# Performance work log

Measured on AMD Instinct MI355X. Metric: run time of the kernel, lower is better.

The kernel has to match this reference:

```python
import jax, jax.numpy as jnp
import numpy as np

B, T, S, F, D, M = 8, 8192, 8192, 64, 64, 128
EPS = 1e-9


def _draw_omega(n_omega, d_feature, rng):
    # Stacked orthogonal blocks scaled by sqrt(d_feature), as in the TF module.
    n_blocks = (n_omega + d_feature - 1) // d_feature + 1
    blocks = []
    for _ in range(n_blocks):
        g = rng.standard_normal((d_feature, d_feature)).astype(np.float32)
        q, _ = np.linalg.qr(g)
        blocks.append(q * np.sqrt(float(d_feature)))
    return jnp.asarray(np.concatenate(blocks, axis=0)[:n_omega])


def setup_inputs() -> dict:
    k0 = jax.random.key(0)
    kq, kv, kk = jax.random.split(k0, 3)
    query = jax.random.normal(kq, (B, T, F), dtype=jnp.float32)
    value = jax.random.normal(kv, (B, S, D), dtype=jnp.float32)
    key = jax.random.normal(kk, (B, S, F), dtype=jnp.float32)
    omega = _draw_omega(M, F, np.random.default_rng(0))  # (M, F)
    return {"query": query, "value": value, "key": key, "omega": omega}


def _phi(x, omega):
    # x: (B, L, F) -> (B, L, 2M) positive random features
    m = omega.shape[0]
    square_sum = jnp.sum(x * x, axis=-1, keepdims=True) / 2.0  # (B, L, 1)
    xw = jnp.einsum('blf,mf->blm', x, omega)                   # (B, L, M)
    unnorm = jnp.exp(jnp.concatenate([xw, -xw], axis=-1) - square_sum) + EPS
    return unnorm / jnp.sqrt(2.0 * m)


def reference(query, value, key, omega):
    q = _phi(query, omega)  # (B, T, 2M)
    k = _phi(key, omega)    # (B, S, 2M)
    ones = jnp.ones(value.shape[:-1] + (1,), dtype=value.dtype)
    v1 = jnp.concatenate([value, ones], axis=-1)               # (B, S, D+1)
    kv = jnp.einsum('bsm,bsd->bmd', k, v1)                     # (B, 2M, D+1)
    qkv = jnp.einsum('btm,bmd->btd', q, kv)                    # (B, T, D+1)
    normalizer = qkv[:, :, -1:]
    return qkv[:, :, :-1] / normalizer
```

## Files before the change

kernel.cpp:

```cpp
#include <hip/hip_runtime.h>


constexpr int NB = 8;
constexpr int NT = 8192;
constexpr float EPSF = 1e-9f;
constexpr float SCALE = 0.0625f;

typedef short s8v __attribute__((ext_vector_type(8)));
typedef short s4v __attribute__((ext_vector_type(4)));
typedef float f4v __attribute__((ext_vector_type(4)));

__device__ inline f4v mfma16(s8v a, s8v b, f4v c) {
  return __builtin_amdgcn_mfma_f32_16x16x32_bf16(a, b, c, 0, 0, 0);
}

__device__ inline short bf16_rne(float f) {
  unsigned u = __builtin_bit_cast(unsigned, f);
  u += 0x7fffu + ((u >> 16) & 1u);
  return (short)(u >> 16);
}
__device__ inline float bf16_to_f(short h) {
  unsigned u = ((unsigned)(unsigned short)h) << 16;
  return __builtin_bit_cast(float, u);
}

__global__ void setup_omega(const float* __restrict__ omega,
                            short* __restrict__ oh, short* __restrict__ ol) {
  int i = blockIdx.x * 256 + threadIdx.x;
  if (i >= 128 * 64) return;
  float w = omega[i];
  short h = bf16_rne(w);
  oh[i] = h;
  ol[i] = bf16_rne(w - bf16_to_f(h));
}

struct PhiRows {
  s8v ah0, al0, ah1, al1;
  float ssr[4];
  float ss;
};

__device__ inline void split8(f4v a, f4v b, s8v& h, s8v& l) {
  float v[8] = {a.x, a.y, a.z, a.w, b.x, b.y, b.z, b.w};
#pragma unroll
  for (int j = 0; j < 8; ++j) {
    short hh = bf16_rne(v[j]);
    h[j] = hh;
    l[j] = bf16_rne(v[j] - bf16_to_f(hh));
  }
}

__device__ inline void load_phi_rows(const float* __restrict__ xrow_base, int lane, PhiRows& P) {
  const int r = lane & 15, q = lane >> 4;
  const float* p = xrow_base + r * 64 + q * 8;
  f4v u0 = *(const f4v*)(p);
  f4v u1 = *(const f4v*)(p + 4);
  f4v u2 = *(const f4v*)(p + 32);
  f4v u3 = *(const f4v*)(p + 36);
  float ss = u0.x * u0.x + u0.y * u0.y + u0.z * u0.z + u0.w * u0.w
           + u1.x * u1.x + u1.y * u1.y + u1.z * u1.z + u1.w * u1.w
           + u2.x * u2.x + u2.y * u2.y + u2.z * u2.z + u2.w * u2.w
           + u3.x * u3.x + u3.y * u3.y + u3.z * u3.z + u3.w * u3.w;
  ss += __shfl_xor(ss, 16, 64);
  ss += __shfl_xor(ss, 32, 64);
  ss *= 0.5f;
  P.ss = ss;
#pragma unroll
  for (int reg = 0; reg < 4; ++reg) P.ssr[reg] = __shfl(ss, q * 4 + reg, 64);
  split8(u0, u1, P.ah0, P.al0);
  split8(u2, u3, P.ah1, P.al1);
}

__device__ inline f4v phi_xw_tile(const PhiRows& P, const short* __restrict__ oh,
                                  const short* __restrict__ ol, int f0, int lane) {
  const int fr = f0 + (lane & 15);
  const int q = lane >> 4;
  s8v bh0 = *(const s8v*)(oh + fr * 64 + q * 8);
  s8v bh1 = *(const s8v*)(oh + fr * 64 + 32 + q * 8);
  s8v bl0 = *(const s8v*)(ol + fr * 64 + q * 8);
  s8v bl1 = *(const s8v*)(ol + fr * 64 + 32 + q * 8);
  f4v c = {0.f, 0.f, 0.f, 0.f};
  c = mfma16(P.ah0, bh0, c);
  c = mfma16(P.ah1, bh1, c);
  c = mfma16(P.al0, bh0, c);
  c = mfma16(P.al1, bh1, c);
  c = mfma16(P.ah0, bl0, c);
  c = mfma16(P.ah1, bl1, c);
  return c;
}

__device__ inline f4v phi_xw_tile_T(const PhiRows& P, const short* __restrict__ oh,
                                    const short* __restrict__ ol, int f0, int lane) {
  const int fr = f0 + (lane & 15);
  const int q = lane >> 4;
  s8v ah0 = *(const s8v*)(oh + fr * 64 + q * 8);
  s8v ah1 = *(const s8v*)(oh + fr * 64 + 32 + q * 8);
  s8v al0 = *(const s8v*)(ol + fr * 64 + q * 8);
  s8v al1 = *(const s8v*)(ol + fr * 64 + 32 + q * 8);
  f4v c = {0.f, 0.f, 0.f, 0.f};
  c = mfma16(ah0, P.ah0, c);
  c = mfma16(ah1, P.ah1, c);
  c = mfma16(al0, P.ah0, c);
  c = mfma16(al1, P.ah1, c);
  c = mfma16(ah0, P.al0, c);
  c = mfma16(ah1, P.al1, c);
  return c;
}

constexpr int KF_P = 72;

__global__ __launch_bounds__(256, 4) void kv_fused(
    const float* __restrict__ key, const float* __restrict__ value,
    const short* __restrict__ oh, const short* __restrict__ ol,
    float* __restrict__ partial, int use_partial) {
  __shared__ short kft[64 * KF_P];
  __shared__ short v1t[80 * KF_P];
  const int tid = threadIdx.x, lane = tid & 63, w = tid >> 6;
  const int b = blockIdx.x >> 8;
  const int cb = blockIdx.x & 255;
  const int chunk = cb >> 2, fq = cb & 3;
  const int s0 = chunk * 128;
  const int q = lane >> 4, r15 = lane & 15;

  for (int i = tid; i < 15 * KF_P; i += 256) v1t[65 * KF_P + i] = 0;

  f4v acc[5];
#pragma unroll
  for (int n = 0; n < 5; ++n) acc[n] = f4v{0.f, 0.f, 0.f, 0.f};

  for (int sc = 0; sc < 2; ++sc) {
    const int sbase = s0 + sc * 64;
    __syncthreads();
    {
      const float* vb = value + ((size_t)b * NT + sbase) * 64;
#pragma unroll
      for (int i = 0; i < 16; ++i) {
        int e = tid + i * 256;
        int s = e >> 6, d = e & 63;
        v1t[d * KF_P + s] = bf16_rne(vb[e]);
      }
      if (tid < 64) v1t[64 * KF_P + tid] = (short)0x3F80;
    }
    {
      PhiRows P;
      load_phi_rows(key + ((size_t)b * NT + sbase + w * 16) * 64, lane, P);
#pragma unroll
      for (int ft = 0; ft < 2; ++ft) {
        f4v c = phi_xw_tile(P, oh, ol, fq * 32 + ft * 16, lane);
        s4v pk, nk;
#pragma unroll
        for (int reg = 0; reg < 4; ++reg) {
          float xw = c[reg];
          pk[reg] = bf16_rne((__expf(xw - P.ssr[reg]) + EPSF) * SCALE);
          nk[reg] = bf16_rne((__expf(-xw - P.ssr[reg]) + EPSF) * SCALE);
        }
        const int scol = w * 16 + q * 4;
        *(s4v*)(kft + (ft * 16 + r15) * KF_P + scol) = pk;
        *(s4v*)(kft + (32 + ft * 16 + r15) * KF_P + scol) = nk;
      }
    }
    __syncthreads();
#pragma unroll
    for (int ks = 0; ks < 2; ++ks) {
      s8v a = *(const s8v*)(kft + (w * 16 + r15) * KF_P + ks * 32 + q * 8);
#pragma unroll
      for (int n = 0; n < 5; ++n) {
        s8v bf = *(const s8v*)(v1t + (n * 16 + r15) * KF_P + ks * 32 + q * 8);
        acc[n] = mfma16(a, bf, acc[n]);
      }
    }
  }
  if (use_partial) {
    float* pb = partial + (size_t)blockIdx.x * 5120;
#pragma unroll
    for (int n = 0; n < 5; ++n) {
      int d = n * 16 + r15;
      *(f4v*)(pb + d * 64 + w * 16 + q * 4) = acc[n];
    }
  } else {
    float* pb = partial + ((size_t)(b * 4 + fq)) * 5120;
#pragma unroll
    for (int n = 0; n < 5; ++n) {
      int d = n * 16 + r15;
#pragma unroll
      for (int reg = 0; reg < 4; ++reg)
        atomicAdd(pb + d * 64 + w * 16 + q * 4 + reg, acc[n][reg]);
    }
  }
}

__global__ __launch_bounds__(256) void kv_finalize(
    const float* __restrict__ src, short* __restrict__ kvfrag,
    int nchunks, size_t bstride) {
  int i = blockIdx.x * 256 + threadIdx.x;
  int b = i / 20480;
  int rem = i - b * 20480;
  int fid = rem >> 9;
  int lane = (rem >> 3) & 63;
  int j = rem & 7;
  int ks = fid / 5, n = fid - ks * 5;
  int r = lane & 15, q = lane >> 4;
  int d = n * 16 + r;
  int k = ks * 32 + q * 8 + j;
  int fq = (k >> 5) & 3;
  int lf = (k & 31) + ((k >> 7) << 5);
  const float* p = src + (size_t)b * bstride + fq * 5120 + d * 64 + lf;
  float s = 0.f;
#pragma unroll 8
  for (int c = 0; c < nchunks; ++c) s += p[(size_t)c * 20480];
  kvfrag[i] = bf16_rne(s);
}

constexpr int QF_P = 264;
__global__ __launch_bounds__(256, 4) void qkv_fused(
    const float* __restrict__ query, const short* __restrict__ oh,
    const short* __restrict__ ol, const short* __restrict__ kvfrag,
    float* __restrict__ out) {
  __shared__ __align__(16) short qf[64 * QF_P];
  const int tid = threadIdx.x, lane = tid & 63, w = tid >> 6;
  const int b = blockIdx.x >> 7;
  const int t0 = (blockIdx.x & 127) * 64;
  const int q = lane >> 4, r15 = lane & 15;

  {
    PhiRows P;
    load_phi_rows(query + ((size_t)b * NT + t0 + w * 16) * 64, lane, P);
    const int t_loc = w * 16 + r15;
#pragma unroll
    for (int ft = 0; ft < 8; ++ft) {
      f4v c = phi_xw_tile_T(P, oh, ol, ft * 16, lane);
      s4v pk, nk;
#pragma unroll
      for (int reg = 0; reg < 4; ++reg) {
        float xw = c[reg];
        pk[reg] = bf16_rne((__expf(xw - P.ss) + EPSF) * SCALE);
        nk[reg] = bf16_rne((__expf(-xw - P.ss) + EPSF) * SCALE);
      }
      *(s4v*)(qf + t_loc * QF_P + ft * 16 + q * 4) = pk;
      *(s4v*)(qf + t_loc * QF_P + 128 + ft * 16 + q * 4) = nk;
    }
  }
  __syncthreads();
  f4v acc[5];
#pragma unroll
  for (int n = 0; n < 5; ++n) acc[n] = f4v{0.f, 0.f, 0.f, 0.f};
  const short* kvb = kvfrag + (size_t)b * 40 * 512;
#pragma unroll
  for (int ks = 0; ks < 8; ++ks) {
    s8v a = *(const s8v*)(qf + (w * 16 + r15) * QF_P + ks * 32 + q * 8);
#pragma unroll
    for (int n = 0; n < 5; ++n) {
      s8v bf = *(const s8v*)(kvb + ((size_t)(ks * 5 + n)) * 512 + lane * 8);
      acc[n] = mfma16(a, bf, acc[n]);
    }
  }
  float den_r[4];
#pragma unroll
  for (int reg = 0; reg < 4; ++reg) den_r[reg] = __shfl(acc[4][reg], lane & 48, 64);
  float* stg = (float*)(qf + w * 16 * QF_P);
#pragma unroll
  for (int n = 0; n < 4; ++n)
#pragma unroll
    for (int reg = 0; reg < 4; ++reg) {
      int row = q * 4 + reg;
      int col = n * 16 + r15;
      stg[row * 68 + col] = acc[n][reg] / den_r[reg];
    }
  float* ob = out + ((size_t)b * NT + t0 + w * 16) * 64;
#pragma unroll
  for (int rr = 0; rr < 4; ++rr) {
    int row = rr * 4 + q;
    int c4 = r15 * 4;
    *(f4v*)(ob + row * 64 + c4) = *(const f4v*)(stg + row * 68 + c4);
  }
}

extern "C" void kernel_launch(void* const* d_in, const int* in_sizes, int n_in,
                              void* d_out, int out_size, void* d_ws, size_t ws_size,
                              hipStream_t stream) {
  const float* query = (const float*)d_in[0];
  const float* value = (const float*)d_in[1];
  const float* key   = (const float*)d_in[2];
  const float* omega = (const float*)d_in[3];
  float* out = (float*)d_out;

  char* ws = (char*)d_ws;
  short* oh = (short*)ws;
  short* ol = (short*)(ws + 16384);
  short* kvfrag = (short*)(ws + 32768);
  float* partial = (float*)(ws + 32768 + 327680);
  const size_t need_full = 32768 + 327680 + (size_t)2048 * 5120 * 4;
  const int use_partial = (ws_size >= need_full) ? 1 : 0;

  setup_omega<<<32, 256, 0, stream>>>(omega, oh, ol);
  if (!use_partial) {
    hipMemsetAsync(partial, 0, (size_t)8 * 4 * 5120 * 4, stream);
  }
  kv_fused<<<2048, 256, 0, stream>>>(key, value, oh, ol, partial, use_partial);
  if (use_partial) {
    kv_finalize<<<640, 256, 0, stream>>>(partial, kvfrag, 64, (size_t)64 * 20480);
  } else {
    kv_finalize<<<640, 256, 0, stream>>>(partial, kvfrag, 1, (size_t)20480);
  }
  qkv_fused<<<1024, 256, 0, stream>>>(query, oh, ol, kvfrag, out);
}
```

Measured before the change: 152.3 us.

## Widen kv_fused feature tiles, store bf16 partials, vectorize value loads

Each kv_fused block now computes 64 of the 128 omega features (two 16-row tiles per wave) instead of 32. This halves the grid and the redundant value loading and transposing, and the value tile is now read with float4 loads. Per-block partial KV sums are stored as bf16 instead of fp32, which cuts partial write and read traffic; kv_finalize is rewritten to match the new layout. A redundant __syncthreads in qkv_fused is dropped because each wave only reads its own LDS rows. The risks are extra rounding from summing bf16 partials and higher register pressure from doubling the accumulators.

```diff
diff --git a/kernel.cpp b/kernel.cpp
--- a/kernel.cpp
+++ b/kernel.cpp
@@ -112,21 +112,23 @@
 __global__ __launch_bounds__(256, 4) void kv_fused(
     const float* __restrict__ key, const float* __restrict__ value,
     const short* __restrict__ oh, const short* __restrict__ ol,
-    float* __restrict__ partial, int use_partial) {
-  __shared__ short kft[64 * KF_P];
+    short* __restrict__ partial, float* __restrict__ kvacc, int use_partial) {
+  __shared__ short kft[128 * KF_P];
   __shared__ short v1t[80 * KF_P];
   const int tid = threadIdx.x, lane = tid & 63, w = tid >> 6;
-  const int b = blockIdx.x >> 8;
-  const int cb = blockIdx.x & 255;
-  const int chunk = cb >> 2, fq = cb & 3;
-  const int s0 = chunk * 128;
+  const int b = blockIdx.x >> 7;
+  const int cb = blockIdx.x & 127;
+  const int fh = cb & 1;
+  const int s0 = (cb >> 1) * 128;
   const int q = lane >> 4, r15 = lane & 15;
 
   for (int i = tid; i < 15 * KF_P; i += 256) v1t[65 * KF_P + i] = 0;
 
-  f4v acc[5];
-#pragma unroll
-  for (int n = 0; n < 5; ++n) acc[n] = f4v{0.f, 0.f, 0.f, 0.f};
+  f4v acc[2][5];
+#pragma unroll
+  for (int j = 0; j < 2; ++j)
+#pragma unroll
+    for (int n = 0; n < 5; ++n) acc[j][n] = f4v{0.f, 0.f, 0.f, 0.f};
 
   for (int sc = 0; sc < 2; ++sc) {
     const int sbase = s0 + sc * 64;
@@ -134,10 +136,14 @@
     {
       const float* vb = value + ((size_t)b * NT + sbase) * 64;
 #pragma unroll
-      for (int i = 0; i < 16; ++i) {
-        int e = tid + i * 256;
-        int s = e >> 6, d = e & 63;
-        v1t[d * KF_P + s] = bf16_rne(vb[e]);
+      for (int i = 0; i < 4; ++i) {
+        int e4 = tid + i * 256;
+        f4v v4 = ((const f4v*)vb)[e4];
+        int s = e4 >> 4, d0 = (e4 & 15) * 4;
+        v1t[(d0 + 0) * KF_P + s] = bf16_rne(v4.x);
+        v1t[(d0 + 1) * KF_P + s] = bf16_rne(v4.y);
+        v1t[(d0 + 2) * KF_P + s] = bf16_rne(v4.z);
+        v1t[(d0 + 3) * KF_P + s] = bf16_rne(v4.w);
       }
       if (tid < 64) v1t[64 * KF_P + tid] = (short)0x3F80;
     }
@@ -145,8 +151,8 @@
       PhiRows P;
       load_phi_rows(key + ((size_t)b * NT + sbase + w * 16) * 64, lane, P);
 #pragma unroll
-      for (int ft = 0; ft < 2; ++ft) {
-        f4v c = phi_xw_tile(P, oh, ol, fq * 32 + ft * 16, lane);
+      for (int ft = 0; ft < 4; ++ft) {
+        f4v c = phi_xw_tile(P, oh, ol, fh * 64 + ft * 16, lane);
         s4v pk, nk;
 #pragma unroll
         for (int reg = 0; reg < 4; ++reg) {
@@ -156,59 +162,78 @@
         }
         const int scol = w * 16 + q * 4;
         *(s4v*)(kft + (ft * 16 + r15) * KF_P + scol) = pk;
-        *(s4v*)(kft + (32 + ft * 16 + r15) * KF_P + scol) = nk;
+        *(s4v*)(kft + (64 + ft * 16 + r15) * KF_P + scol) = nk;
       }
     }
     __syncthreads();
 #pragma unroll
     for (int ks = 0; ks < 2; ++ks) {
-      s8v a = *(const s8v*)(kft + (w * 16 + r15) * KF_P + ks * 32 + q * 8);
+      s8v bf[5];
+#pragma unroll
+      for (int n = 0; n < 5; ++n)
+        bf[n] = *(const s8v*)(v1t + (n * 16 + r15) * KF_P + ks * 32 + q * 8);
+#pragma unroll
+      for (int j = 0; j < 2; ++j) {
+        s8v a = *(const s8v*)(kft + (w * 32 + j * 16 + r15) * KF_P + ks * 32 + q * 8);
+#pragma unroll
+        for (int n = 0; n < 5; ++n) acc[j][n] = mfma16(a, bf[n], acc[j][n]);
+      }
+    }
+  }
+  if (use_partial) {
+    short* pb = partial + (size_t)blockIdx.x * (80 * 128);
+#pragma unroll
+    for (int j = 0; j < 2; ++j)
 #pragma unroll
       for (int n = 0; n < 5; ++n) {
-        s8v bf = *(const s8v*)(v1t + (n * 16 + r15) * KF_P + ks * 32 + q * 8);
-        acc[n] = mfma16(a, bf, acc[n]);
-      }
-    }
-  }
-  if (use_partial) {
-    float* pb = partial + (size_t)blockIdx.x * 5120;
-#pragma unroll
-    for (int n = 0; n < 5; ++n) {
-      int d = n * 16 + r15;
-      *(f4v*)(pb + d * 64 + w * 16 + q * 4) = acc[n];
-    }
+        int d = n * 16 + r15;
+        int lf = w * 32 + j * 16 + q * 4;
+        s4v pk;
+#pragma unroll
+        for (int reg = 0; reg < 4; ++reg) pk[reg] = bf16_rne(acc[j][n][reg]);
+        *(s4v*)(pb + d * 128 + lf) = pk;
+      }
   } else {
-    float* pb = partial + ((size_t)(b * 4 + fq)) * 5120;
-#pragma unroll
-    for (int n = 0; n < 5; ++n) {
-      int d = n * 16 + r15;
-#pragma unroll
-      for (int reg = 0; reg < 4; ++reg)
-        atomicAdd(pb + d * 64 + w * 16 + q * 4 + reg, acc[n][reg]);
-    }
+    float* pb = kvacc + (size_t)b * (80 * 256);
+#pragma unroll
+    for (int j = 0; j < 2; ++j)
+#pragma unroll
+      for (int n = 0; n < 5; ++n) {
+        int d = n * 16 + r15;
+        int lf = w * 32 + j * 16 + q * 4;
+#pragma unroll
+        for (int reg = 0; reg < 4; ++reg) {
+          int lfx = lf + reg;
+          int m = ((lfx & 63) + fh * 64) + 128 * (lfx >> 6);
+          atomicAdd(pb + d * 256 + m, acc[j][n][reg]);
+        }
+      }
   }
 }
 
 __global__ __launch_bounds__(256) void kv_finalize(
-    const float* __restrict__ src, short* __restrict__ kvfrag,
-    int nchunks, size_t bstride) {
+    const short* __restrict__ partial, const float* __restrict__ kvacc,
+    short* __restrict__ kvfrag, int use_partial) {
   int i = blockIdx.x * 256 + threadIdx.x;
   int b = i / 20480;
   int rem = i - b * 20480;
-  int fid = rem >> 9;
-  int lane = (rem >> 3) & 63;
-  int j = rem & 7;
-  int ks = fid / 5, n = fid - ks * 5;
-  int r = lane & 15, q = lane >> 4;
-  int d = n * 16 + r;
-  int k = ks * 32 + q * 8 + j;
-  int fq = (k >> 5) & 3;
-  int lf = (k & 31) + ((k >> 7) << 5);
-  const float* p = src + (size_t)b * bstride + fq * 5120 + d * 64 + lf;
+  int d = rem >> 8;
+  int m = rem & 255;
   float s = 0.f;
+  if (use_partial) {
+    int o = m & 127, sg = m >> 7;
+    int fh = o >> 6;
+    int lf = (o & 63) + (sg << 6);
+    const short* p = partial + ((size_t)(b * 128 + fh)) * (80 * 128) + d * 128 + lf;
 #pragma unroll 8
-  for (int c = 0; c < nchunks; ++c) s += p[(size_t)c * 20480];
-  kvfrag[i] = bf16_rne(s);
+    for (int c = 0; c < 64; ++c) s += bf16_to_f(p[(size_t)c * 2 * (80 * 128)]);
+  } else {
+    s = kvacc[(size_t)(b * 80 + d) * 256 + m];
+  }
+  int ks = m >> 5, qq = (m >> 3) & 3, j = m & 7;
+  int n = d >> 4, r = d & 15;
+  int lane = qq * 16 + r;
+  kvfrag[(((size_t)b * 40 + ks * 5 + n) * 64 + lane) * 8 + j] = bf16_rne(s);
 }
 
 constexpr int QF_P = 264;
@@ -240,7 +265,6 @@
       *(s4v*)(qf + t_loc * QF_P + 128 + ft * 16 + q * 4) = nk;
     }
   }
-  __syncthreads();
   f4v acc[5];
 #pragma unroll
   for (int n = 0; n < 5; ++n) acc[n] = f4v{0.f, 0.f, 0.f, 0.f};
@@ -288,19 +312,16 @@
   short* oh = (short*)ws;
   short* ol = (short*)(ws + 16384);
   short* kvfrag = (short*)(ws + 32768);
-  float* partial = (float*)(ws + 32768 + 327680);
-  const size_t need_full = 32768 + 327680 + (size_t)2048 * 5120 * 4;
+  short* partial = (short*)(ws + 360448);
+  float* kvacc = (float*)(ws + 360448);
+  const size_t need_full = 360448 + (size_t)1024 * 80 * 128 * 2;
   const int use_partial = (ws_size >= need_full) ? 1 : 0;
 
   setup_omega<<<32, 256, 0, stream>>>(omega, oh, ol);
   if (!use_partial) {
-    hipMemsetAsync(partial, 0, (size_t)8 * 4 * 5120 * 4, stream);
-  }
-  kv_fused<<<2048, 256, 0, stream>>>(key, value, oh, ol, partial, use_partial);
-  if (use_partial) {
-    kv_finalize<<<640, 256, 0, stream>>>(partial, kvfrag, 64, (size_t)64 * 20480);
-  } else {
-    kv_finalize<<<640, 256, 0, stream>>>(partial, kvfrag, 1, (size_t)20480);
-  }
+    hipMemsetAsync(kvacc, 0, (size_t)8 * 80 * 256 * 4, stream);
+  }
+  kv_fused<<<1024, 256, 0, stream>>>(key, value, oh, ol, partial, kvacc, use_partial);
+  kv_finalize<<<640, 256, 0, stream>>>(partial, kvacc, kvfrag, use_partial);
   qkv_fused<<<1024, 256, 0, stream>>>(query, oh, ol, kvfrag, out);
 }
```

Measured after the change: 143.3 us. -5.9%, faster.
